# Optimization experiments

Hardware: AMD Instinct MI355X
Metric: run time of the kernel (lower is better)

## Reference

```python
import jax, jax.numpy as jnp
import numpy as np

NF, IN_NF, N_LAYERS = 64, 196, 3
B, H, W = 1, 256, 256
P3 = [(1, 1), (1, 1)]
P1 = [(0, 0), (0, 0)]


def conv2d(x, w, pad):
    return jax.lax.conv_general_dilated(x, w, (1, 1), pad,
                                        dimension_numbers=('NCHW', 'OIHW', 'NCHW'))


def prelu(x, a):
    return jnp.where(x >= 0, x, a[None, :, None, None] * x)


def warp(x, flow):
    # standard backward bilinear warp, zero padding outside the image
    Bx, C, Hx, Wx = x.shape
    yy, xx = jnp.meshgrid(jnp.arange(Hx, dtype=x.dtype),
                          jnp.arange(Wx, dtype=x.dtype), indexing='ij')
    px = xx[None] + flow[:, 0]  # (B,H,W)
    py = yy[None] + flow[:, 1]

    def sample(img, px, py):  # img (C,H,W); px,py (H,W)
        x0 = jnp.floor(px)
        y0 = jnp.floor(py)
        x1 = x0 + 1.0
        y1 = y0 + 1.0
        wx1 = px - x0
        wx0 = 1.0 - wx1
        wy1 = py - y0
        wy0 = 1.0 - wy1

        def gather(xi, yi):
            valid = (xi >= 0) & (xi <= Wx - 1) & (yi >= 0) & (yi <= Hx - 1)
            xc = jnp.clip(xi, 0, Wx - 1).astype(jnp.int32)
            yc = jnp.clip(yi, 0, Hx - 1).astype(jnp.int32)
            return img[:, yc, xc] * valid.astype(img.dtype)

        return (gather(x0, y0) * (wx0 * wy0) + gather(x1, y0) * (wx1 * wy0)
                + gather(x0, y1) * (wx0 * wy1) + gather(x1, y1) * (wx1 * wy1))

    return jax.vmap(sample)(x, px, py)


def setup_inputs() -> dict:
    key = jax.random.key(0)
    ks = jax.random.split(key, 11)
    s = 0.05
    return {
        'feat_0': jax.random.normal(ks[0], (B, 64, H, W), jnp.float32),
        'feat_1': jax.random.normal(ks[1], (B, 64, H, W), jnp.float32),
        'feat_dense': jax.random.normal(ks[2], (B, 64, H, W), jnp.float32),
        'flow': jax.random.normal(ks[3], (B, 4, H, W), jnp.float32),
        'space_mask': jax.random.uniform(ks[4], (B, 1, H, W), jnp.float32),
        'head_w': jax.random.normal(ks[5], (IN_NF, IN_NF, 3, 3), jnp.float32) * s,
        'head_a': jnp.full((IN_NF,), 0.25, jnp.float32),
        'conv_w': jax.random.normal(ks[6], (N_LAYERS, IN_NF, IN_NF, 3, 3), jnp.float32) * s,
        'conv_a': jnp.full((N_LAYERS, IN_NF), 0.25, jnp.float32),
        'last_w': jax.random.normal(ks[7], (4 + NF, IN_NF * (N_LAYERS + 1), 1, 1), jnp.float32) * s,
        'last_b': jax.random.normal(ks[8], (4 + NF,), jnp.float32) * s,
        'mask_w': jax.random.normal(ks[9], (2, NF, 3, 3), jnp.float32) * s,
        'mask_b': jax.random.normal(ks[10], (2,), jnp.float32) * s,
    }


def reference(feat_0, feat_1, feat_dense, flow, space_mask,
              head_w, head_a, conv_w, conv_a, last_w, last_b, mask_w, mask_b):
    f0 = warp(feat_0, flow[:, :2])
    f1 = warp(feat_1, flow[:, 2:4])
    x = jnp.concatenate([f0, f1, feat_dense, flow], axis=1)  # (B, in_nf, H, W)
    sm_up = jnp.repeat(jnp.repeat(space_mask, 2, axis=2), 2, axis=3)

    # head: conv3x3 -> PReLU, then mask (dense / use_sparsity=False path)
    x = prelu(conv2d(x, head_w, P3), head_a) * space_mask
    outs = [x]
    for i in range(N_LAYERS):
        x = conv2d(x, conv_w[i], P3) * space_mask
        x = prelu(x, conv_a[i])
        outs.append(x)
    x = conv2d(jnp.concatenate(outs, axis=1), last_w, P1) + last_b[None, :, None, None]

    smn = conv2d(x[:, 4:], mask_w, P3) + mask_b[None, :, None, None]

    Bx, Cx, Hx, Wx = x.shape
    x_up = jax.image.resize(x, (Bx, Cx, 2 * Hx, 2 * Wx), method='bilinear')
    smn_up = jax.image.resize(smn, (Bx, 2, 2 * Hx, 2 * Wx), method='bilinear')

    flow_out = x_up[:, :4]
    feat_t = x_up[:, 4:]
    # eval-mode mask (training=False): hard argmax between channel 0 and 1
    mask_next = (smn_up[:, :1] > smn_up[:, 1:2]).astype(x.dtype) * sm_up
    return flow_out, feat_t, mask_next
```

## Files before the change

### kernel.cpp

```cpp
#include <hip/hip_runtime.h>

typedef _Float16 f16;
typedef _Float16 f16x8 __attribute__((ext_vector_type(8)));
typedef _Float16 f16x4 __attribute__((ext_vector_type(4)));
typedef float    f32x4 __attribute__((ext_vector_type(4)));

#define MFMA16(a,b,c) __builtin_amdgcn_mfma_f32_16x16x32_f16(a,b,c,0,0,0)

#define NPIX 65536
#define CSTR 448
#define RB   (256*CSTR*2)
#define SBUF ((size_t)258*256*CSTR*2)

#define PK_OB   1024
#define PK_CB   14336
#define PK_TAP  100352
#define PK_CONV 903168
#define PKL_CB  5120
#define PKL_BI  35840

#define STG_BYTES 16640
#define STG_CHUNKS 1040

__global__ void k_pack_conv(const float* __restrict__ head_w,
                            const float* __restrict__ conv_w,
                            f16* __restrict__ dst)
{
    int t = blockIdx.x*256 + threadIdx.x;
    if (t >= 4*9*7*14*2*64) return;
    int lane = t & 63; t >>= 6;
    int sel  = t & 1;  t >>= 1;
    int ob   = t % 14; t /= 14;
    int cb   = t % 7;  t /= 7;
    int tap  = t % 9;  t /= 9;
    int li   = t;
    const float* W = (li == 0) ? head_w : (conv_w + (size_t)(li-1)*196*196*9);
    int oc  = ob*16 + (lane & 15);
    int ic0 = cb*32 + (lane >> 4)*8;
    f16x8 v;
#pragma unroll
    for (int j = 0; j < 8; ++j) {
        int ic = ic0 + j;
        float x = 0.f;
        if (oc < 196 && ic < 196) x = W[((size_t)oc*196 + ic)*9 + tap];
        f16 h = (f16)x;
        v[j] = (sel == 0) ? h : (f16)(x - (float)h);
    }
    *(f16x8*)(dst + (size_t)li*PK_CONV +
              (((size_t)((tap*7+cb)*14 + ob)*2 + sel)*64 + lane)*8) = v;
}

__global__ void k_pack_last(const float* __restrict__ last_w, f16* __restrict__ dst)
{
    int t = blockIdx.x*256 + threadIdx.x;
    if (t >= 4*7*5*2*64) return;
    int lane = t & 63; t >>= 6;
    int sel  = t & 1;  t >>= 1;
    int ob   = t % 5;  t /= 5;
    int cb   = t % 7;  t /= 7;
    int bi   = t;
    int oc = ob*16 + (lane & 15);
    int k0 = cb*32 + (lane >> 4)*8;
    f16x8 v;
#pragma unroll
    for (int j = 0; j < 8; ++j) {
        int k = k0 + j;
        float x = 0.f;
        if (oc < 68 && k < 196) x = last_w[(size_t)oc*784 + bi*196 + k];
        f16 h = (f16)x;
        v[j] = (sel == 0) ? h : (f16)(x - (float)h);
    }
    *(f16x8*)(dst + (((size_t)((bi*7+cb)*5 + ob)*2 + sel)*64 + lane)*8) = v;
}

struct Gath { int o00,o01,o10,o11; float w00,w01,w10,w11; };

__device__ inline Gath mk_gath(float pxf, float pyf)
{
    float x0 = floorf(pxf), y0 = floorf(pyf);
    float x1 = x0 + 1.f, y1 = y0 + 1.f;
    float wx1 = pxf - x0, wx0 = 1.f - wx1;
    float wy1 = pyf - y0, wy0 = 1.f - wy1;
    bool vx0 = (x0 >= 0.f) && (x0 <= 255.f);
    bool vx1 = (x1 >= 0.f) && (x1 <= 255.f);
    bool vy0 = (y0 >= 0.f) && (y0 <= 255.f);
    bool vy1 = (y1 >= 0.f) && (y1 <= 255.f);
    int ix0 = min(max((int)x0, 0), 255);
    int ix1 = min(max((int)x1, 0), 255);
    int iy0 = min(max((int)y0, 0), 255);
    int iy1 = min(max((int)y1, 0), 255);
    Gath g;
    g.o00 = iy0*256 + ix0; g.w00 = (vx0 && vy0) ? wx0*wy0 : 0.f;
    g.o01 = iy0*256 + ix1; g.w01 = (vx1 && vy0) ? wx1*wy0 : 0.f;
    g.o10 = iy1*256 + ix0; g.w10 = (vx0 && vy1) ? wx0*wy1 : 0.f;
    g.o11 = iy1*256 + ix1; g.w11 = (vx1 && vy1) ? wx1*wy1 : 0.f;
    return g;
}

__device__ inline void store4(f16* __restrict__ op, int c0,
                              float a, float b, float c, float d)
{
    f16x4 hi, lo;
    f16 h;
    h = (f16)a; hi[0] = h; lo[0] = (f16)(a - (float)h);
    h = (f16)b; hi[1] = h; lo[1] = (f16)(b - (float)h);
    h = (f16)c; hi[2] = h; lo[2] = (f16)(c - (float)h);
    h = (f16)d; hi[3] = h; lo[3] = (f16)(d - (float)h);
    f16* p = op + (c0 >> 5)*64 + (c0 & 31);
    *(f16x4*)p        = hi;
    *(f16x4*)(p + 32) = lo;
}

__global__ void k_warp_concat(const float* __restrict__ f0, const float* __restrict__ f1,
                              const float* __restrict__ fd, const float* __restrict__ flow,
                              f16* __restrict__ out)
{
    int px = blockIdx.x*256 + threadIdx.x;
    int row = px >> 8, col = px & 255;
    f16* op = out + ((size_t)(row+1)*256 + col)*CSTR;
    Gath g0 = mk_gath((float)col + flow[px],          (float)row + flow[NPIX   + px]);
    Gath g1 = mk_gath((float)col + flow[2*NPIX + px], (float)row + flow[3*NPIX + px]);
#pragma unroll
    for (int c = 0; c < 64; c += 4) {
        float v[4];
#pragma unroll
        for (int r = 0; r < 4; ++r) {
            const float* im = f0 + (size_t)(c+r)*NPIX;
            v[r] = g0.w00*im[g0.o00] + g0.w01*im[g0.o01] + g0.w10*im[g0.o10] + g0.w11*im[g0.o11];
        }
        store4(op, c, v[0], v[1], v[2], v[3]);
    }
#pragma unroll
    for (int c = 0; c < 64; c += 4) {
        float v[4];
#pragma unroll
        for (int r = 0; r < 4; ++r) {
            const float* im = f1 + (size_t)(c+r)*NPIX;
            v[r] = g1.w00*im[g1.o00] + g1.w01*im[g1.o01] + g1.w10*im[g1.o10] + g1.w11*im[g1.o11];
        }
        store4(op, 64 + c, v[0], v[1], v[2], v[3]);
    }
#pragma unroll
    for (int c = 0; c < 64; c += 4) {
        store4(op, 128 + c, fd[(size_t)(c+0)*NPIX + px], fd[(size_t)(c+1)*NPIX + px],
                            fd[(size_t)(c+2)*NPIX + px], fd[(size_t)(c+3)*NPIX + px]);
    }
    store4(op, 192, flow[px], flow[NPIX+px], flow[2*NPIX+px], flow[3*NPIX+px]);
#pragma unroll
    for (int c = 196; c < 224; c += 4) store4(op, c, 0.f, 0.f, 0.f, 0.f);
}

__global__ __launch_bounds__(448, 4)
void k_conv3x3(const f16* __restrict__ in, f16* __restrict__ out,
               const f16* __restrict__ pack, const float* __restrict__ alpha,
               const float* __restrict__ mask)
{
    __shared__ __align__(16) char bs[2*STG_BYTES];

    int bid = blockIdx.x;
    int wg  = (bid & 7)*64 + (bid >> 3);
    int row  = wg >> 1;
    int col0 = (wg & 1) << 7;

    int tid  = threadIdx.x;
    int lane = tid & 63;
    int w    = tid >> 6;
    int l15  = lane & 15, lk = lane >> 4;

    f32x4 acc[2][8];
#pragma unroll
    for (int o = 0; o < 2; ++o)
#pragma unroll
        for (int pb = 0; pb < 8; ++pb)
            acc[o][pb] = (f32x4){0.f,0.f,0.f,0.f};

    const f16x8 Z8 = {(f16)0,(f16)0,(f16)0,(f16)0,(f16)0,(f16)0,(f16)0,(f16)0};

    f16x8 sr[3];
    int ccap[3];
#pragma unroll
    for (int u = 0; u < 3; ++u) ccap[u] = tid + u*448;

    {
#pragma unroll
        for (int u = 0; u < 3; ++u) {
            int c = ccap[u];
            f16x8 v = Z8;
            if (c < STG_CHUNKS) {
                int p = c >> 3, sl = c & 7;
                int cp = col0 - 1 + p;
                if ((unsigned)cp < 256u)
                    v = *(const f16x8*)(in + ((size_t)row*256 + cp)*CSTR + sl*8);
            }
            sr[u] = v;
        }
#pragma unroll
        for (int u = 0; u < 3; ++u) {
            int c = ccap[u];
            if (c < STG_CHUNKS) {
                int p = c >> 3, sl = c & 7;
                *(f16x8*)(bs + p*128 + ((sl ^ (p & 7)) << 4)) = sr[u];
            }
        }
    }
    __syncthreads();

    for (int idx = 0; idx < 21; ++idx) {
        int ky = idx / 7;
        int cb = idx - ky*7;

        int nidx = idx + 1;
        if (nidx < 21) {
            int nky = nidx / 7;
            int ncb = nidx - nky*7;
#pragma unroll
            for (int u = 0; u < 3; ++u) {
                int c = ccap[u];
                f16x8 v = Z8;
                if (c < STG_CHUNKS) {
                    int p = c >> 3, sl = c & 7;
                    int cp = col0 - 1 + p;
                    if ((unsigned)cp < 256u)
                        v = *(const f16x8*)(in + ((size_t)(row+nky)*256 + cp)*CSTR + ncb*64 + sl*8);
                }
                sr[u] = v;
            }
        }

        const char* bufc = bs + (idx & 1)*STG_BYTES;
#pragma unroll
        for (int kx = 0; kx < 3; ++kx) {
            const f16* ap = pack + ((size_t)(((ky*3+kx)*7 + cb)*14 + 2*w)*2)*512 + (size_t)lane*8;
            f16x8 ah0 = *(const f16x8*)(ap);
            f16x8 al0 = *(const f16x8*)(ap + 512);
            f16x8 ah1 = *(const f16x8*)(ap + 1024);
            f16x8 al1 = *(const f16x8*)(ap + 1536);
            int t = l15 + kx;
            int sz = t & 7;
            int hoff = t*128 + ((lk ^ sz) << 4);
            int loff = t*128 + (((4+lk) ^ sz) << 4);
#pragma unroll
            for (int pb = 0; pb < 8; ++pb) {
                f16x8 bh = *(const f16x8*)(bufc + hoff + pb*2048);
                f16x8 bl = *(const f16x8*)(bufc + loff + pb*2048);
                acc[0][pb] = MFMA16(ah0, bh, acc[0][pb]);
                acc[0][pb] = MFMA16(ah0, bl, acc[0][pb]);
                acc[0][pb] = MFMA16(al0, bh, acc[0][pb]);
                acc[1][pb] = MFMA16(ah1, bh, acc[1][pb]);
                acc[1][pb] = MFMA16(ah1, bl, acc[1][pb]);
                acc[1][pb] = MFMA16(al1, bh, acc[1][pb]);
            }
        }

        if (nidx < 21) {
            char* bufn = bs + (nidx & 1)*STG_BYTES;
#pragma unroll
            for (int u = 0; u < 3; ++u) {
                int c = ccap[u];
                if (c < STG_CHUNKS) {
                    int p = c >> 3, sl = c & 7;
                    *(f16x8*)(bufn + p*128 + ((sl ^ (p & 7)) << 4)) = sr[u];
                }
            }
        }
        __syncthreads();
    }

    float mv[8];
#pragma unroll
    for (int pb = 0; pb < 8; ++pb) mv[pb] = mask[row*256 + col0 + pb*16 + l15];
#pragma unroll
    for (int o = 0; o < 2; ++o) {
        int oc0 = (2*w + o)*16 + lk*4;
        f32x4 a4 = *(const f32x4*)(alpha + min(oc0, 192));
#pragma unroll
        for (int pb = 0; pb < 8; ++pb) {
            f32x4 d = acc[o][pb];
            f16x4 hi, lo;
#pragma unroll
            for (int r = 0; r < 4; ++r) {
                float v = d[r];
                v = (v >= 0.f ? v : a4[r]*v) * mv[pb];
                f16 h = (f16)v;
                hi[r] = h;
                lo[r] = (f16)(v - (float)h);
            }
            f16* op = out + ((size_t)(row+1)*256 + col0 + pb*16 + l15)*CSTR + (oc0 >> 5)*64 + (oc0 & 31);
            *(f16x4*)op        = hi;
            *(f16x4*)(op + 32) = lo;
        }
    }
}

__global__ __launch_bounds__(256, 4)
void k_acc_last(const f16* __restrict__ in, const f16* __restrict__ pack,
                const float* __restrict__ bias, float* __restrict__ accp, int bi)
{
    int lane = threadIdx.x & 63;
    int wid  = (blockIdx.x << 2) | (threadIdx.x >> 6);
    int row  = wid >> 3;
    int col0 = (wid & 7) << 5;
    int l15 = lane & 15, lk = lane >> 4;

    f32x4 acc[5][2];
#pragma unroll
    for (int i = 0; i < 5; ++i)
#pragma unroll
        for (int j = 0; j < 2; ++j)
            acc[i][j] = (f32x4){0.f, 0.f, 0.f, 0.f};

    const f16* bb = in + ((size_t)(row+1)*256 + col0 + l15)*CSTR + lk*8;
    const f16* ap = pack + (size_t)bi*PKL_BI + (size_t)lane*8;
    for (int cb = 0; cb < 7; ++cb) {
        f16x8 bh[2], bl[2];
#pragma unroll
        for (int pb = 0; pb < 2; ++pb) {
            const f16* p = bb + (size_t)pb*(16*CSTR) + cb*64;
            bh[pb] = *(const f16x8*)p;
            bl[pb] = *(const f16x8*)(p + 32);
        }
        const f16* a = ap + cb*PKL_CB;
#pragma unroll
        for (int ob = 0; ob < 5; ++ob) {
            f16x8 ah = *(const f16x8*)(a + ob*1024);
            f16x8 al = *(const f16x8*)(a + ob*1024 + 512);
#pragma unroll
            for (int pb = 0; pb < 2; ++pb) {
                acc[ob][pb] = MFMA16(ah, bh[pb], acc[ob][pb]);
                acc[ob][pb] = MFMA16(ah, bl[pb], acc[ob][pb]);
                acc[ob][pb] = MFMA16(al, bh[pb], acc[ob][pb]);
            }
        }
    }
#pragma unroll
    for (int ob = 0; ob < 5; ++ob) {
        int oc0 = ob*16 + lk*4;
#pragma unroll
        for (int pb = 0; pb < 2; ++pb) {
            int px = row*256 + col0 + pb*16 + l15;
            float* dst = accp + (size_t)px*80 + oc0;
            f32x4 d = acc[ob][pb];
            if (bi == 0) {
                f32x4 b4;
#pragma unroll
                for (int r = 0; r < 4; ++r) b4[r] = bias[min(oc0 + r, 67)];
                *(f32x4*)dst = d + b4;
            } else {
                *(f32x4*)dst = *(const f32x4*)dst + d;
            }
        }
    }
}

__global__ void k_smn(const float* __restrict__ accp, const float* __restrict__ mw,
                      const float* __restrict__ mb, float* __restrict__ smn)
{
    int px = blockIdx.x*256 + threadIdx.x;
    int row = px >> 8, col = px & 255;
    float s0 = mb[0], s1 = mb[1];
    for (int ky = 0; ky < 3; ++ky) {
        int r = row + ky - 1;
        if ((unsigned)r > 255u) continue;
        for (int kx = 0; kx < 3; ++kx) {
            int c = col + kx - 1;
            if ((unsigned)c > 255u) continue;
            const float* ab = accp + ((size_t)r*256 + c)*80 + 4;
            const float* w  = mw + ky*3 + kx;
#pragma unroll
            for (int ch = 0; ch < 64; ch += 4) {
                f32x4 v = *(const f32x4*)(ab + ch);
                s0 += v[0]*w[(ch+0)*9] + v[1]*w[(ch+1)*9] + v[2]*w[(ch+2)*9] + v[3]*w[(ch+3)*9];
                s1 += v[0]*w[(64+ch+0)*9] + v[1]*w[(64+ch+1)*9] + v[2]*w[(64+ch+2)*9] + v[3]*w[(64+ch+3)*9];
            }
        }
    }
    smn[px]        = s0;
    smn[NPIX + px] = s1;
}

__global__ void k_upsample(const float* __restrict__ accp, float* __restrict__ outp)
{
    int o = blockIdx.x*256 + threadIdx.x;
    int oy = o >> 9, ox = o & 511;
    int my = oy >> 1, mx = ox >> 1;
    int r0, r1, c0, c1; float wy0, wy1, wx0, wx1;
    if (oy & 1) { r0 = my;            r1 = min(my+1, 255); wy0 = 0.75f; wy1 = 0.25f; }
    else        { r0 = max(my-1, 0);  r1 = my;             wy0 = 0.25f; wy1 = 0.75f; }
    if (ox & 1) { c0 = mx;            c1 = min(mx+1, 255); wx0 = 0.75f; wx1 = 0.25f; }
    else        { c0 = max(mx-1, 0);  c1 = mx;             wx0 = 0.25f; wx1 = 0.75f; }
    const float* p00 = accp + ((size_t)r0*256 + c0)*80;
    const float* p01 = accp + ((size_t)r0*256 + c1)*80;
    const float* p10 = accp + ((size_t)r1*256 + c0)*80;
    const float* p11 = accp + ((size_t)r1*256 + c1)*80;
    float w00 = wy0*wx0, w01 = wy0*wx1, w10 = wy1*wx0, w11 = wy1*wx1;
#pragma unroll
    for (int ch = 0; ch < 68; ch += 4) {
        f32x4 va = *(const f32x4*)(p00 + ch);
        f32x4 vb = *(const f32x4*)(p01 + ch);
        f32x4 vc = *(const f32x4*)(p10 + ch);
        f32x4 vd = *(const f32x4*)(p11 + ch);
        f32x4 v;
#pragma unroll
        for (int r = 0; r < 4; ++r)
            v[r] = w00*va[r] + w01*vb[r] + w10*vc[r] + w11*vd[r];
        outp[(size_t)(ch+0)*262144 + o] = v[0];
        outp[(size_t)(ch+1)*262144 + o] = v[1];
        outp[(size_t)(ch+2)*262144 + o] = v[2];
        outp[(size_t)(ch+3)*262144 + o] = v[3];
    }
}

__global__ void k_mask(const float* __restrict__ smn, const float* __restrict__ sm,
                       float* __restrict__ outp)
{
    int o = blockIdx.x*256 + threadIdx.x;
    int oy = o >> 9, ox = o & 511;
    int my = oy >> 1, mx = ox >> 1;
    int r0, r1, c0, c1; float wy0, wy1, wx0, wx1;
    if (oy & 1) { r0 = my;            r1 = min(my+1, 255); wy0 = 0.75f; wy1 = 0.25f; }
    else        { r0 = max(my-1, 0);  r1 = my;             wy0 = 0.25f; wy1 = 0.75f; }
    if (ox & 1) { c0 = mx;            c1 = min(mx+1, 255); wx0 = 0.75f; wx1 = 0.25f; }
    else        { c0 = max(mx-1, 0);  c1 = mx;             wx0 = 0.25f; wx1 = 0.75f; }
    float w00 = wy0*wx0, w01 = wy0*wx1, w10 = wy1*wx0, w11 = wy1*wx1;
    int i00 = r0*256 + c0, i01 = r0*256 + c1, i10 = r1*256 + c0, i11 = r1*256 + c1;
    float s0 = w00*smn[i00] + w01*smn[i01] + w10*smn[i10] + w11*smn[i11];
    float s1 = w00*smn[NPIX+i00] + w01*smn[NPIX+i01] + w10*smn[NPIX+i10] + w11*smn[NPIX+i11];
    outp[(size_t)68*262144 + o] = (s0 > s1) ? sm[my*256 + mx] : 0.f;
}

extern "C" void kernel_launch(void* const* d_in, const int* in_sizes, int n_in,
                              void* d_out, int out_size, void* d_ws, size_t ws_size,
                              hipStream_t stream)
{
    const float* feat0  = (const float*)d_in[0];
    const float* feat1  = (const float*)d_in[1];
    const float* featd  = (const float*)d_in[2];
    const float* flow   = (const float*)d_in[3];
    const float* smask  = (const float*)d_in[4];
    const float* head_w = (const float*)d_in[5];
    const float* head_a = (const float*)d_in[6];
    const float* conv_w = (const float*)d_in[7];
    const float* conv_a = (const float*)d_in[8];
    const float* last_w = (const float*)d_in[9];
    const float* last_b = (const float*)d_in[10];
    const float* mask_w = (const float*)d_in[11];
    const float* mask_b = (const float*)d_in[12];
    float* outp = (float*)d_out;

    char* ws = (char*)d_ws;
    size_t off = 4096;
    f16* bufA = (f16*)(ws + off); off += SBUF + 4096;
    f16* bufB = (f16*)(ws + off); off += SBUF + 4096;
    f16* packc = (f16*)(ws + off); off += (size_t)4*PK_CONV*2;
    f16* packl = (f16*)(ws + off); off += (size_t)4*PKL_BI*2;
    float* accp = (float*)(ws + off); off += (size_t)NPIX*80*4;
    float* smn  = (float*)(ws + off); off += (size_t)2*NPIX*4;

    hipMemsetAsync(bufA, 0, RB, stream);
    hipMemsetAsync((char*)bufA + (size_t)257*RB, 0, RB, stream);
    hipMemsetAsync(bufB, 0, RB, stream);
    hipMemsetAsync((char*)bufB + (size_t)257*RB, 0, RB, stream);

    k_pack_conv<<<1764, 256, 0, stream>>>(head_w, conv_w, packc);
    k_pack_last<<<70, 256, 0, stream>>>(last_w, packl);
    k_warp_concat<<<256, 256, 0, stream>>>(feat0, feat1, featd, flow, bufA);

    k_conv3x3<<<512, 448, 0, stream>>>(bufA, bufB, packc, head_a, smask);
    k_acc_last<<<512, 256, 0, stream>>>(bufB, packl, last_b, accp, 0);
    k_conv3x3<<<512, 448, 0, stream>>>(bufB, bufA, packc + (size_t)1*PK_CONV, conv_a, smask);
    k_acc_last<<<512, 256, 0, stream>>>(bufA, packl, last_b, accp, 1);
    k_conv3x3<<<512, 448, 0, stream>>>(bufA, bufB, packc + (size_t)2*PK_CONV, conv_a + 196, smask);
    k_acc_last<<<512, 256, 0, stream>>>(bufB, packl, last_b, accp, 2);
    k_conv3x3<<<512, 448, 0, stream>>>(bufB, bufA, packc + (size_t)3*PK_CONV, conv_a + 392, smask);
    k_acc_last<<<512, 256, 0, stream>>>(bufA, packl, last_b, accp, 3);

    k_smn<<<256, 256, 0, stream>>>(accp, mask_w, mask_b, smn);
    k_upsample<<<1024, 256, 0, stream>>>(accp, outp);
    k_mask<<<1024, 256, 0, stream>>>(smn, smask, outp);
}
```

Baseline: 830.6 us.

## Restructure conv3x3 with direct global-to-LDS staging and 8-wave output/pixel split

The 3x3 conv kernel now stages input tiles with global_load_lds, which writes straight into shared memory and removes the register round-trip. Out-of-range and padding pixels read from a zeroed scratch page. Work is split across 8 waves: each covers 7 output-channel blocks and 32 pixels instead of 2 channel blocks and 128 pixels, and s_setprio raises priority around the MFMA section. This changes the weight/activation reuse balance: each wave now loads more weight fragments per step but fewer LDS activation fragments, and it runs more waves per block.

Measured after the change: 896.3 us. +7.9%, slower.

```diff
diff --git a/kernel.cpp b/kernel.cpp
--- a/kernel.cpp
+++ b/kernel.cpp
@@ -19,8 +19,7 @@
 #define PKL_CB  5120
 #define PKL_BI  35840
 
-#define STG_BYTES 16640
-#define STG_CHUNKS 1040
+#define STG_BYTES 17408
 
 __global__ void k_pack_conv(const float* __restrict__ head_w,
                             const float* __restrict__ conv_w,
@@ -150,10 +149,10 @@
     for (int c = 196; c < 224; c += 4) store4(op, c, 0.f, 0.f, 0.f, 0.f);
 }
 
-__global__ __launch_bounds__(448, 4)
+__global__ __launch_bounds__(512, 4)
 void k_conv3x3(const f16* __restrict__ in, f16* __restrict__ out,
                const f16* __restrict__ pack, const float* __restrict__ alpha,
-               const float* __restrict__ mask)
+               const float* __restrict__ mask, const f16* __restrict__ zp)
 {
     __shared__ __align__(16) char bs[2*STG_BYTES];
 
@@ -166,115 +165,88 @@
     int lane = tid & 63;
     int w    = tid >> 6;
     int l15  = lane & 15, lk = lane >> 4;
-
-    f32x4 acc[2][8];
-#pragma unroll
-    for (int o = 0; o < 2; ++o)
-#pragma unroll
-        for (int pb = 0; pb < 8; ++pb)
+    int och7   = (w & 1)*7;
+    int pxbase = (w >> 1)*32;
+
+    f32x4 acc[7][2];
+#pragma unroll
+    for (int o = 0; o < 7; ++o)
+#pragma unroll
+        for (int pb = 0; pb < 2; ++pb)
             acc[o][pb] = (f32x4){0.f,0.f,0.f,0.f};
 
-    const f16x8 Z8 = {(f16)0,(f16)0,(f16)0,(f16)0,(f16)0,(f16)0,(f16)0,(f16)0};
-
-    f16x8 sr[3];
-    int ccap[3];
-#pragma unroll
-    for (int u = 0; u < 3; ++u) ccap[u] = tid + u*448;
-
-    {
+    auto stage = [&](char* bufn, int ky, int cb) {
 #pragma unroll
         for (int u = 0; u < 3; ++u) {
-            int c = ccap[u];
-            f16x8 v = Z8;
-            if (c < STG_CHUNKS) {
-                int p = c >> 3, sl = c & 7;
+            int j = u*8 + w;
+            if (j < 17) {
+                int p  = j*8 + (lane >> 3);
+                int sl = lane & 7;
                 int cp = col0 - 1 + p;
-                if ((unsigned)cp < 256u)
-                    v = *(const f16x8*)(in + ((size_t)row*256 + cp)*CSTR + sl*8);
-            }
-            sr[u] = v;
-        }
-#pragma unroll
-        for (int u = 0; u < 3; ++u) {
-            int c = ccap[u];
-            if (c < STG_CHUNKS) {
-                int p = c >> 3, sl = c & 7;
-                *(f16x8*)(bs + p*128 + ((sl ^ (p & 7)) << 4)) = sr[u];
-            }
-        }
-    }
+                const f16* src;
+                if (p < 130 && (unsigned)cp < 256u)
+                    src = in + ((size_t)(row+ky)*256 + cp)*CSTR + cb*64 + ((sl ^ (p & 7)) * 8);
+                else
+                    src = zp + lane*8;
+                __builtin_amdgcn_global_load_lds(
+                    (const __attribute__((address_space(1))) void*)src,
+                    (__attribute__((address_space(3))) void*)(bufn + j*1024),
+                    16, 0, 0);
+            }
+        }
+    };
+
+    stage(bs, 0, 0);
     __syncthreads();
 
     for (int idx = 0; idx < 21; ++idx) {
         int ky = idx / 7;
         int cb = idx - ky*7;
-
         int nidx = idx + 1;
         if (nidx < 21) {
             int nky = nidx / 7;
-            int ncb = nidx - nky*7;
-#pragma unroll
-            for (int u = 0; u < 3; ++u) {
-                int c = ccap[u];
-                f16x8 v = Z8;
-                if (c < STG_CHUNKS) {
-                    int p = c >> 3, sl = c & 7;
-                    int cp = col0 - 1 + p;
-                    if ((unsigned)cp < 256u)
-                        v = *(const f16x8*)(in + ((size_t)(row+nky)*256 + cp)*CSTR + ncb*64 + sl*8);
+            stage(bs + (nidx & 1)*STG_BYTES, nky, nidx - nky*7);
+        }
+
+        const char* bufc = bs + (idx & 1)*STG_BYTES;
+        __builtin_amdgcn_s_setprio(1);
+#pragma unroll
+        for (int kx = 0; kx < 3; ++kx) {
+            const f16* ap = pack + ((size_t)(((ky*3+kx)*7 + cb)*14 + och7))*1024 + (size_t)lane*8;
+            f16x8 bh[2], bl[2];
+#pragma unroll
+            for (int pb = 0; pb < 2; ++pb) {
+                int t = pxbase + pb*16 + l15 + kx;
+                int sz = t & 7;
+                const char* base = bufc + t*128;
+                bh[pb] = *(const f16x8*)(base + ((lk ^ sz) << 4));
+                bl[pb] = *(const f16x8*)(base + (((4+lk) ^ sz) << 4));
+            }
+#pragma unroll
+            for (int o = 0; o < 7; ++o) {
+                f16x8 ah = *(const f16x8*)(ap + o*1024);
+                f16x8 al = *(const f16x8*)(ap + o*1024 + 512);
+#pragma unroll
+                for (int pb = 0; pb < 2; ++pb) {
+                    acc[o][pb] = MFMA16(ah, bh[pb], acc[o][pb]);
+                    acc[o][pb] = MFMA16(ah, bl[pb], acc[o][pb]);
+                    acc[o][pb] = MFMA16(al, bh[pb], acc[o][pb]);
                 }
-                sr[u] = v;
-            }
-        }
-
-        const char* bufc = bs + (idx & 1)*STG_BYTES;
-#pragma unroll
-        for (int kx = 0; kx < 3; ++kx) {
-            const f16* ap = pack + ((size_t)(((ky*3+kx)*7 + cb)*14 + 2*w)*2)*512 + (size_t)lane*8;
-            f16x8 ah0 = *(const f16x8*)(ap);
-            f16x8 al0 = *(const f16x8*)(ap + 512);
-            f16x8 ah1 = *(const f16x8*)(ap + 1024);
-            f16x8 al1 = *(const f16x8*)(ap + 1536);
-            int t = l15 + kx;
-            int sz = t & 7;
-            int hoff = t*128 + ((lk ^ sz) << 4);
-            int loff = t*128 + (((4+lk) ^ sz) << 4);
-#pragma unroll
-            for (int pb = 0; pb < 8; ++pb) {
-                f16x8 bh = *(const f16x8*)(bufc + hoff + pb*2048);
-                f16x8 bl = *(const f16x8*)(bufc + loff + pb*2048);
-                acc[0][pb] = MFMA16(ah0, bh, acc[0][pb]);
-                acc[0][pb] = MFMA16(ah0, bl, acc[0][pb]);
-                acc[0][pb] = MFMA16(al0, bh, acc[0][pb]);
-                acc[1][pb] = MFMA16(ah1, bh, acc[1][pb]);
-                acc[1][pb] = MFMA16(ah1, bl, acc[1][pb]);
-                acc[1][pb] = MFMA16(al1, bh, acc[1][pb]);
-            }
-        }
-
-        if (nidx < 21) {
-            char* bufn = bs + (nidx & 1)*STG_BYTES;
-#pragma unroll
-            for (int u = 0; u < 3; ++u) {
-                int c = ccap[u];
-                if (c < STG_CHUNKS) {
-                    int p = c >> 3, sl = c & 7;
-                    *(f16x8*)(bufn + p*128 + ((sl ^ (p & 7)) << 4)) = sr[u];
-                }
-            }
-        }
+            }
+        }
+        __builtin_amdgcn_s_setprio(0);
         __syncthreads();
     }
 
-    float mv[8];
-#pragma unroll
-    for (int pb = 0; pb < 8; ++pb) mv[pb] = mask[row*256 + col0 + pb*16 + l15];
-#pragma unroll
-    for (int o = 0; o < 2; ++o) {
-        int oc0 = (2*w + o)*16 + lk*4;
+    float mv[2];
+#pragma unroll
+    for (int pb = 0; pb < 2; ++pb) mv[pb] = mask[row*256 + col0 + pxbase + pb*16 + l15];
+#pragma unroll
+    for (int o = 0; o < 7; ++o) {
+        int oc0 = och7*16 + o*16 + lk*4;
         f32x4 a4 = *(const f32x4*)(alpha + min(oc0, 192));
 #pragma unroll
-        for (int pb = 0; pb < 8; ++pb) {
+        for (int pb = 0; pb < 2; ++pb) {
             f32x4 d = acc[o][pb];
             f16x4 hi, lo;
 #pragma unroll
@@ -285,7 +257,8 @@
                 hi[r] = h;
                 lo[r] = (f16)(v - (float)h);
             }
-            f16* op = out + ((size_t)(row+1)*256 + col0 + pb*16 + l15)*CSTR + (oc0 >> 5)*64 + (oc0 & 31);
+            f16* op = out + ((size_t)(row+1)*256 + col0 + pxbase + pb*16 + l15)*CSTR
+                          + (oc0 >> 5)*64 + (oc0 & 31);
             *(f16x4*)op        = hi;
             *(f16x4*)(op + 32) = lo;
         }
@@ -448,7 +421,8 @@
     float* outp = (float*)d_out;
 
     char* ws = (char*)d_ws;
-    size_t off = 4096;
+    size_t off = 0;
+    f16* zp = (f16*)(ws + off); off += 4096;
     f16* bufA = (f16*)(ws + off); off += SBUF + 4096;
     f16* bufB = (f16*)(ws + off); off += SBUF + 4096;
     f16* packc = (f16*)(ws + off); off += (size_t)4*PK_CONV*2;
@@ -456,6 +430,7 @@
     float* accp = (float*)(ws + off); off += (size_t)NPIX*80*4;
     float* smn  = (float*)(ws + off); off += (size_t)2*NPIX*4;
 
+    hipMemsetAsync(zp, 0, 4096, stream);
     hipMemsetAsync(bufA, 0, RB, stream);
     hipMemsetAsync((char*)bufA + (size_t)257*RB, 0, RB, stream);
     hipMemsetAsync(bufB, 0, RB, stream);
@@ -465,13 +440,13 @@
     k_pack_last<<<70, 256, 0, stream>>>(last_w, packl);
     k_warp_concat<<<256, 256, 0, stream>>>(feat0, feat1, featd, flow, bufA);
 
-    k_conv3x3<<<512, 448, 0, stream>>>(bufA, bufB, packc, head_a, smask);
+    k_conv3x3<<<512, 512, 0, stream>>>(bufA, bufB, packc, head_a, smask, zp);
     k_acc_last<<<512, 256, 0, stream>>>(bufB, packl, last_b, accp, 0);
-    k_conv3x3<<<512, 448, 0, stream>>>(bufB, bufA, packc + (size_t)1*PK_CONV, conv_a, smask);
+    k_conv3x3<<<512, 512, 0, stream>>>(bufB, bufA, packc + (size_t)1*PK_CONV, conv_a, smask, zp);
     k_acc_last<<<512, 256, 0, stream>>>(bufA, packl, last_b, accp, 1);
-    k_conv3x3<<<512, 448, 0, stream>>>(bufA, bufB, packc + (size_t)2*PK_CONV, conv_a + 196, smask);
+    k_conv3x3<<<512, 512, 0, stream>>>(bufA, bufB, packc + (size_t)2*PK_CONV, conv_a + 196, smask, zp);
     k_acc_last<<<512, 256, 0, stream>>>(bufB, packl, last_b, accp, 2);
-    k_conv3x3<<<512, 448, 0, stream>>>(bufB, bufA, packc + (size_t)3*PK_CONV, conv_a + 392, smask);
+    k_conv3x3<<<512, 512, 0, stream>>>(bufB, bufA, packc + (size_t)3*PK_CONV, conv_a + 392, smask, zp);
     k_acc_last<<<512, 256, 0, stream>>>(bufA, packl, last_b, accp, 3);
 
     k_smn<<<256, 256, 0, stream>>>(accp, mask_w, mask_b, smn);
```
